# Kernel tuning notes

Hardware: AMD Instinct MI355X
Metric: run time of the kernel (lower is better)

Reference implementation:

```python
import jax, jax.numpy as jnp
import numpy as np
import math

B, C, N = 8, 512, 2048

def setup_inputs() -> dict:
    key = jax.random.key(0)
    ks = jax.random.split(key, 7)
    s = 0.02
    return {
        "x": jax.random.normal(ks[0], (B, C, N), dtype=jnp.float32),
        "Wq": jax.random.normal(ks[1], (C // 2, C), dtype=jnp.float32) * s,
        "bq": jax.random.normal(ks[2], (C // 2,), dtype=jnp.float32) * s,
        "Wk": jax.random.normal(ks[3], (C // 2, C), dtype=jnp.float32) * s,
        "bk": jax.random.normal(ks[4], (C // 2,), dtype=jnp.float32) * s,
        "Wv": jax.random.normal(ks[5], (C, C), dtype=jnp.float32) * s,
        "bv": jax.random.normal(ks[6], (C,), dtype=jnp.float32) * s,
    }

def reference(x, Wq, bq, Wk, bk, Wv, bv):
    # pointwise conv1d == channel matmul: (O,C) x (B,C,N) -> (B,O,N)
    Q = jnp.einsum('oc,bcn->bon', Wq, x) + bq[None, :, None]  # (B, C/2, N)
    K = jnp.einsum('oc,bcn->bon', Wk, x) + bk[None, :, None]  # (B, C/2, N)
    V = jnp.einsum('oc,bcn->bon', Wv, x) + bv[None, :, None]  # (B, C, N)
    scale = 1.0 / math.sqrt(K.shape[1])
    A = jnp.einsum('bcn,bcm->bnm', Q, K) * scale              # (B, N, N)
    A = jax.nn.softmax(A, axis=-1)
    out = jnp.einsum('bcm,bnm->bcn', V, A)                    # V @ A^T
    return x + out
```

## Files before the change

### kernel.cpp

```cpp
#include <hip/hip_runtime.h>

#define B_ 8
#define C_ 512
#define N_ 2048
#define O_ 256

typedef unsigned short u16;
typedef unsigned char u8;
typedef unsigned int uint;
typedef float f32x4 __attribute__((ext_vector_type(4)));
typedef int i32x8 __attribute__((ext_vector_type(8)));

#define AS1 __attribute__((address_space(1)))
#define AS3 __attribute__((address_space(3)))

__device__ __forceinline__ u16 f2bf(float f) {
  union { float f; unsigned u; } v; v.f = f;
  return (u16)((v.u + 0x7fffu + ((v.u >> 16) & 1u)) >> 16);
}
__device__ __forceinline__ float bf2f(u16 h) {
  union { uint u; float f; } v; v.u = ((uint)h) << 16; return v.f;
}
__device__ __forceinline__ uint pk4_e4m3(float a, float b, float c, float d) {
  int r = __builtin_amdgcn_cvt_pk_fp8_f32(a, b, 0, false);
  r = __builtin_amdgcn_cvt_pk_fp8_f32(c, d, r, true);
  return (uint)r;
}

union MxFrag { i32x8 v; uint4 q[2]; };

__device__ __forceinline__ void mx_mainloop(
    const u8* __restrict__ Ag, int lda,
    const u8* __restrict__ Bg, int ldb, int K,
    u8 (&As)[128][128], u8 (&Bs)[128][128], f32x4 (&acc)[4][4])
{
  const int t = threadIdx.x;
  const int lane = t & 63;
  const int w = t >> 6;
  const int wm = (w >> 1) * 64, wn = (w & 1) * 64;
  const int lrow = lane & 15, quad = lane >> 4;
  const int swz = lrow & 7;
  const int r8 = lane >> 3;
  const int gsrc = (lane & 7) ^ r8;

  for (int k0 = 0; k0 < K; k0 += 128) {
#pragma unroll
    for (int i = 0; i < 4; i++) {
      int row = i * 32 + w * 8;
      __builtin_amdgcn_global_load_lds(
          (const AS1 uint*)(Ag + (size_t)(row + r8) * lda + k0 + gsrc * 16),
          (AS3 uint*)(&As[row][0]), 16, 0, 0);
      __builtin_amdgcn_global_load_lds(
          (const AS1 uint*)(Bg + (size_t)(row + r8) * ldb + k0 + gsrc * 16),
          (AS3 uint*)(&Bs[row][0]), 16, 0, 0);
    }
    __syncthreads();
    const int g0 = (quad * 2) ^ swz, g1 = (quad * 2 + 1) ^ swz;
    MxFrag af[4], bfr[4];
#pragma unroll
    for (int i = 0; i < 4; i++) {
      const u8* rp = &As[wm + i * 16 + lrow][0];
      af[i].q[0] = *(const uint4*)(rp + g0 * 16);
      af[i].q[1] = *(const uint4*)(rp + g1 * 16);
    }
#pragma unroll
    for (int j = 0; j < 4; j++) {
      const u8* rp = &Bs[wn + j * 16 + lrow][0];
      bfr[j].q[0] = *(const uint4*)(rp + g0 * 16);
      bfr[j].q[1] = *(const uint4*)(rp + g1 * 16);
    }
#pragma unroll
    for (int i = 0; i < 4; i++)
#pragma unroll
      for (int j = 0; j < 4; j++)
        acc[i][j] = __builtin_amdgcn_mfma_scale_f32_16x16x128_f8f6f4(
            af[i].v, bfr[j].v, acc[i][j],
            0, 0,
            0, 0x7f7f7f7f,
            0, 0x7f7f7f7f);
    __syncthreads();
  }
}

__global__ __launch_bounds__(256) void prep_kernel(
    const float* __restrict__ x,
    const float* __restrict__ Wq, const float* __restrict__ Wk,
    const float* __restrict__ Wv,
    u8* __restrict__ xT8, u8* __restrict__ Wq8, u8* __restrict__ Wk8,
    u8* __restrict__ Wv8, float* __restrict__ rowsum)
{
  __shared__ u16 tile[64][72];
  const int bid = blockIdx.x;
  const int t = threadIdx.x;
  if (bid < 2048) {
    int b = bid >> 8;
    int n0 = (bid & 31) * 64;
    int c0 = ((bid >> 5) & 7) * 64;
    const float* src = x + (size_t)b * C_ * N_ + (size_t)c0 * N_ + n0;
    int r = t >> 4;
    int f4 = (t & 15) * 4;
#pragma unroll
    for (int i = 0; i < 4; i++) {
      int c = r + 16 * i;
      float4 v = *(const float4*)(src + (size_t)c * N_ + f4);
      tile[f4 + 0][c] = f2bf(v.x);
      tile[f4 + 1][c] = f2bf(v.y);
      tile[f4 + 2][c] = f2bf(v.z);
      tile[f4 + 3][c] = f2bf(v.w);
    }
    __syncthreads();
    u8* dst = xT8 + (size_t)b * N_ * C_ + (size_t)n0 * C_ + c0;
    int n = t >> 2;
    int cc = (t & 3) * 16;
    uint4 d;
    d.x = pk4_e4m3(bf2f(tile[n][cc + 0]), bf2f(tile[n][cc + 1]),
                   bf2f(tile[n][cc + 2]), bf2f(tile[n][cc + 3]));
    d.y = pk4_e4m3(bf2f(tile[n][cc + 4]), bf2f(tile[n][cc + 5]),
                   bf2f(tile[n][cc + 6]), bf2f(tile[n][cc + 7]));
    d.z = pk4_e4m3(bf2f(tile[n][cc + 8]), bf2f(tile[n][cc + 9]),
                   bf2f(tile[n][cc + 10]), bf2f(tile[n][cc + 11]));
    d.w = pk4_e4m3(bf2f(tile[n][cc + 12]), bf2f(tile[n][cc + 13]),
                   bf2f(tile[n][cc + 14]), bf2f(tile[n][cc + 15]));
    *(uint4*)(dst + (size_t)n * C_ + cc) = d;
  } else {
    int gid = (bid - 2048) * 256 + t;
    const float* src; u8* dst; int o;
    if (gid < 32768)      { src = Wq; dst = Wq8; o = gid; }
    else if (gid < 65536) { src = Wk; dst = Wk8; o = gid - 32768; }
    else                  { src = Wv; dst = Wv8; o = gid - 65536; }
    float4 v = *(const float4*)(src + (size_t)o * 4);
    *(uint*)(dst + (size_t)o * 4) = pk4_e4m3(v.x, v.y, v.z, v.w);
    if (gid < 4096) {
      float4 z = {0.f, 0.f, 0.f, 0.f};
      *(float4*)(rowsum + gid * 4) = z;
    }
  }
}

__global__ __launch_bounds__(256) void proj_all_kernel(
    const u8* __restrict__ xT8,
    const u8* __restrict__ Wq8, const float* __restrict__ bq,
    const u8* __restrict__ Wk8, const float* __restrict__ bk,
    const u8* __restrict__ Wv8, const float* __restrict__ bv,
    u8* __restrict__ Qt8, u8* __restrict__ Kt8, u8* __restrict__ V8)
{
  __shared__ __align__(16) u8 As[128][128], Bs[128][128];
  const int n0 = blockIdx.x * 128;
  const int b = blockIdx.y;
  const int sub = blockIdx.z;
  const u8* xTb = xT8 + (size_t)b * N_ * C_ + (size_t)n0 * C_;

  const f32x4 zero = {0.f, 0.f, 0.f, 0.f};
  f32x4 acc[4][4];
#pragma unroll
  for (int i = 0; i < 4; i++)
#pragma unroll
    for (int j = 0; j < 4; j++) acc[i][j] = zero;

  const int lane = threadIdx.x & 63;
  const int w = threadIdx.x >> 6;
  const int wm = (w >> 1) * 64, wn = (w & 1) * 64;
  const int quad = lane >> 4, lcol = lane & 15;

  if (sub < 4) {
    const int isK = sub >> 1;
    const int o0 = (sub & 1) * 128;
    const u8* Wg = (isK ? Wk8 : Wq8) + (size_t)o0 * C_;
    const float* bias = isK ? bk : bq;
    u8* outp = (isK ? Kt8 : Qt8) + (size_t)b * N_ * O_;

    mx_mainloop(Wg, C_, xTb, C_, C_, As, Bs, acc);

#pragma unroll
    for (int i = 0; i < 4; i++) {
      int obase = o0 + wm + i * 16 + quad * 4;
      float4 bb = *(const float4*)(bias + obase);
#pragma unroll
      for (int j = 0; j < 4; j++) {
        int n = n0 + wn + j * 16 + lcol;
        uint d = pk4_e4m3(acc[i][j][0] + bb.x, acc[i][j][1] + bb.y,
                          acc[i][j][2] + bb.z, acc[i][j][3] + bb.w);
        *(uint*)(outp + (size_t)n * O_ + obase) = d;
      }
    }
  } else {
    const int c0 = (sub - 4) * 128;
    const u8* Wg = Wv8 + (size_t)c0 * C_;
    u8* outp = V8 + (size_t)b * C_ * N_;

    mx_mainloop(xTb, C_, Wg, C_, C_, As, Bs, acc);

#pragma unroll
    for (int j = 0; j < 4; j++) {
      int c = c0 + wn + j * 16 + lcol;
      float bb = bv[c];
#pragma unroll
      for (int i = 0; i < 4; i++) {
        int nbase = n0 + wm + i * 16 + quad * 4;
        uint d = pk4_e4m3(acc[i][j][0] + bb, acc[i][j][1] + bb,
                          acc[i][j][2] + bb, acc[i][j][3] + bb);
        *(uint*)(outp + (size_t)c * N_ + nbase) = d;
      }
    }
  }
}

__global__ __launch_bounds__(256) void attn_s_kernel(
    const u8* __restrict__ Qt8, const u8* __restrict__ Kt8,
    u8* __restrict__ P, float* __restrict__ rowsum)
{
  __shared__ __align__(16) u8 As[128][128], Bs[128][128];
  int b = blockIdx.z;
  int m0 = blockIdx.x * 128, n0 = blockIdx.y * 128;
  const u8* Ag = Kt8 + (size_t)b * N_ * O_ + (size_t)m0 * O_;
  const u8* Bg = Qt8 + (size_t)b * N_ * O_ + (size_t)n0 * O_;

  const f32x4 zero = {0.f, 0.f, 0.f, 0.f};
  f32x4 acc[4][4];
#pragma unroll
  for (int i = 0; i < 4; i++)
#pragma unroll
    for (int j = 0; j < 4; j++) acc[i][j] = zero;

  mx_mainloop(Ag, O_, Bg, O_, O_, As, Bs, acc);

  u8* Pp = P + (size_t)b * N_ * N_;
  float* rs = rowsum + (size_t)b * N_;
  const int lane = threadIdx.x & 63;
  const int w = threadIdx.x >> 6;
  const int wm = (w >> 1) * 64, wn = (w & 1) * 64;
  const int quad = lane >> 4, lcol = lane & 15;

  float partial[4];
#pragma unroll
  for (int j = 0; j < 4; j++) partial[j] = 0.f;

#pragma unroll
  for (int j = 0; j < 4; j++) {
    int n = n0 + wn + j * 16 + lcol;
#pragma unroll
    for (int i = 0; i < 4; i++) {
      int mbase = m0 + wm + i * 16 + quad * 4;
      float p0 = __expf(acc[i][j][0] * 0.0625f);
      float p1 = __expf(acc[i][j][1] * 0.0625f);
      float p2 = __expf(acc[i][j][2] * 0.0625f);
      float p3 = __expf(acc[i][j][3] * 0.0625f);
      *(uint*)(Pp + (size_t)n * N_ + mbase) = pk4_e4m3(p0, p1, p2, p3);
      partial[j] += p0 + p1 + p2 + p3;
    }
  }
#pragma unroll
  for (int msk = 16; msk < 64; msk <<= 1)
#pragma unroll
    for (int j = 0; j < 4; j++)
      partial[j] += __shfl_xor(partial[j], msk);
  if (quad == 0) {
#pragma unroll
    for (int j = 0; j < 4; j++)
      atomicAdd(&rs[n0 + wn + j * 16 + lcol], partial[j]);
  }
}

__global__ __launch_bounds__(256) void attn_o_kernel(
    const u8* __restrict__ V, const u8* __restrict__ P,
    const float* __restrict__ rowsum, const float* __restrict__ x,
    float* __restrict__ out)
{
  __shared__ __align__(16) u8 As[64][128], Bs[128][128];
  const int b = blockIdx.z;
  const int c0 = blockIdx.y * 64, n0 = blockIdx.x * 128;
  const u8* Ag = V + (size_t)b * C_ * N_ + (size_t)c0 * N_;
  const u8* Bg = P + (size_t)b * N_ * N_ + (size_t)n0 * N_;

  const int t = threadIdx.x;
  const int lane = t & 63;
  const int w = t >> 6;
  const int wm = (w >> 1) * 32;
  const int wn = (w & 1) * 64;
  const int lrow = lane & 15, quad = lane >> 4;
  const int swz = lrow & 7;
  const int r8 = lane >> 3;
  const int gsrc = (lane & 7) ^ r8;

  const f32x4 zero = {0.f, 0.f, 0.f, 0.f};
  f32x4 acc[2][4];
#pragma unroll
  for (int i = 0; i < 2; i++)
#pragma unroll
    for (int j = 0; j < 4; j++) acc[i][j] = zero;

  for (int k0 = 0; k0 < N_; k0 += 128) {
#pragma unroll
    for (int s = 0; s < 2; s++) {
      int row = (w * 2 + s) * 8;
      __builtin_amdgcn_global_load_lds(
          (const AS1 uint*)(Ag + (size_t)(row + r8) * N_ + k0 + gsrc * 16),
          (AS3 uint*)(&As[row][0]), 16, 0, 0);
    }
#pragma unroll
    for (int s = 0; s < 4; s++) {
      int row = (w * 4 + s) * 8;
      __builtin_amdgcn_global_load_lds(
          (const AS1 uint*)(Bg + (size_t)(row + r8) * N_ + k0 + gsrc * 16),
          (AS3 uint*)(&Bs[row][0]), 16, 0, 0);
    }
    __syncthreads();
    const int g0 = (quad * 2) ^ swz, g1 = (quad * 2 + 1) ^ swz;
    MxFrag af[2], bfr[4];
#pragma unroll
    for (int i = 0; i < 2; i++) {
      const u8* rp = &As[wm + i * 16 + lrow][0];
      af[i].q[0] = *(const uint4*)(rp + g0 * 16);
      af[i].q[1] = *(const uint4*)(rp + g1 * 16);
    }
#pragma unroll
    for (int j = 0; j < 4; j++) {
      const u8* rp = &Bs[wn + j * 16 + lrow][0];
      bfr[j].q[0] = *(const uint4*)(rp + g0 * 16);
      bfr[j].q[1] = *(const uint4*)(rp + g1 * 16);
    }
#pragma unroll
    for (int i = 0; i < 2; i++)
#pragma unroll
      for (int j = 0; j < 4; j++)
        acc[i][j] = __builtin_amdgcn_mfma_scale_f32_16x16x128_f8f6f4(
            af[i].v, bfr[j].v, acc[i][j],
            0, 0, 0, 0x7f7f7f7f, 0, 0x7f7f7f7f);
    __syncthreads();
  }

  const float* xb = x + (size_t)b * C_ * N_;
  float* ob = out + (size_t)b * C_ * N_;
  float invl[4];
#pragma unroll
  for (int j = 0; j < 4; j++)
    invl[j] = 1.f / rowsum[b * N_ + n0 + wn + j * 16 + lrow];

#pragma unroll
  for (int i = 0; i < 2; i++)
#pragma unroll
    for (int rr = 0; rr < 4; rr++) {
      int c = c0 + wm + i * 16 + quad * 4 + rr;
#pragma unroll
      for (int j = 0; j < 4; j++) {
        int n = n0 + wn + j * 16 + lrow;
        size_t idx = (size_t)c * N_ + n;
        ob[idx] = xb[idx] + acc[i][j][rr] * invl[j];
      }
    }
}

extern "C" void kernel_launch(void* const* d_in, const int* in_sizes, int n_in,
                              void* d_out, int out_size, void* d_ws, size_t ws_size,
                              hipStream_t stream)
{
  (void)in_sizes; (void)n_in; (void)out_size; (void)ws_size;
  const float* x  = (const float*)d_in[0];
  const float* Wq = (const float*)d_in[1];
  const float* bq = (const float*)d_in[2];
  const float* Wk = (const float*)d_in[3];
  const float* bk = (const float*)d_in[4];
  const float* Wv = (const float*)d_in[5];
  const float* bv = (const float*)d_in[6];
  float* out = (float*)d_out;

  char* ws = (char*)d_ws;
  size_t off = 0;
  auto carve = [&](size_t bytes) -> char* {
    char* p = ws + off;
    off += (bytes + 255) & ~(size_t)255;
    return p;
  };
  u8*  xT8  = (u8*) carve((size_t)B_ * N_ * C_);
  u8*  Wq8  = (u8*) carve((size_t)O_ * C_);
  u8*  Wk8  = (u8*) carve((size_t)O_ * C_);
  u8*  Wv8  = (u8*) carve((size_t)C_ * C_);
  u8*  Qt8  = (u8*) carve((size_t)B_ * N_ * O_);
  u8*  Kt8  = (u8*) carve((size_t)B_ * N_ * O_);
  u8*  Vb   = (u8*) carve((size_t)B_ * C_ * N_);
  u8*  P    = (u8*) carve((size_t)B_ * N_ * N_);
  float* rowsum = (float*)carve((size_t)B_ * N_ * 4);

  prep_kernel<<<dim3(2560), 256, 0, stream>>>(
      x, Wq, Wk, Wv, xT8, Wq8, Wk8, Wv8, rowsum);
  proj_all_kernel<<<dim3(N_ / 128, B_, 8), 256, 0, stream>>>(
      xT8, Wq8, bq, Wk8, bk, Wv8, bv, Qt8, Kt8, Vb);
  attn_s_kernel<<<dim3(N_ / 128, N_ / 128, B_), 256, 0, stream>>>(Qt8, Kt8, P, rowsum);
  attn_o_kernel<<<dim3(N_ / 128, C_ / 64, B_), 256, 0, stream>>>(Vb, P, rowsum, x, out);
}
```

Measured before the change: 169.1 us.

## Double-buffer LDS tiles with async global-to-LDS prefetch in all GEMM kernels

Replaces the single-buffered load/sync/compute loops with a shared double-buffered mainloop. The next K tile is prefetched into LDS with global_load_lds while the current one is computed, using explicit vmcnt waits and raw barriers. This is meant to hide global memory latency behind MFMA work in the projection, score and output kernels. In exchange, LDS use per block doubles, which may lower occupancy, and correctness now depends on hand-placed waitcnt counts.

After: 177.5 us. 4.9% more time.

```diff
diff --git a/kernel.cpp b/kernel.cpp
--- a/kernel.cpp
+++ b/kernel.cpp
@@ -29,56 +29,91 @@
 
 union MxFrag { i32x8 v; uint4 q[2]; };
 
-__device__ __forceinline__ void mx_mainloop(
+template<int AR>
+__device__ __forceinline__ void mx_stage_tile(
     const u8* __restrict__ Ag, int lda,
-    const u8* __restrict__ Bg, int ldb, int K,
-    u8 (&As)[128][128], u8 (&Bs)[128][128], f32x4 (&acc)[4][4])
+    const u8* __restrict__ Bg, int ldb, int k0,
+    u8 (&As)[AR][128], u8 (&Bs)[128][128], int w, int r8, int gsrc)
+{
+#pragma unroll
+  for (int s = 0; s < AR / 32; s++) {
+    int row = (w * (AR / 32) + s) * 8;
+    __builtin_amdgcn_global_load_lds(
+        (const AS1 uint*)(Ag + (size_t)(row + r8) * lda + k0 + gsrc * 16),
+        (AS3 uint*)(&As[row][0]), 16, 0, 0);
+  }
+#pragma unroll
+  for (int s = 0; s < 4; s++) {
+    int row = (w * 4 + s) * 8;
+    __builtin_amdgcn_global_load_lds(
+        (const AS1 uint*)(Bg + (size_t)(row + r8) * ldb + k0 + gsrc * 16),
+        (AS3 uint*)(&Bs[row][0]), 16, 0, 0);
+  }
+}
+
+template<int MI, int AR>
+__device__ __forceinline__ void mx_compute_tile(
+    const u8 (&As)[AR][128], const u8 (&Bs)[128][128],
+    f32x4 (&acc)[MI][4], int wm, int wn, int lrow, int quad)
+{
+  const int swz = lrow & 7;
+  const int g0 = (quad * 2) ^ swz, g1 = (quad * 2 + 1) ^ swz;
+  MxFrag af[MI], bfr[4];
+#pragma unroll
+  for (int i = 0; i < MI; i++) {
+    const u8* rp = &As[wm + i * 16 + lrow][0];
+    af[i].q[0] = *(const uint4*)(rp + g0 * 16);
+    af[i].q[1] = *(const uint4*)(rp + g1 * 16);
+  }
+#pragma unroll
+  for (int j = 0; j < 4; j++) {
+    const u8* rp = &Bs[wn + j * 16 + lrow][0];
+    bfr[j].q[0] = *(const uint4*)(rp + g0 * 16);
+    bfr[j].q[1] = *(const uint4*)(rp + g1 * 16);
+  }
+  asm volatile("s_waitcnt lgkmcnt(0)" ::: "memory");
+#pragma unroll
+  for (int i = 0; i < MI; i++)
+#pragma unroll
+    for (int j = 0; j < 4; j++)
+      acc[i][j] = __builtin_amdgcn_mfma_scale_f32_16x16x128_f8f6f4(
+          af[i].v, bfr[j].v, acc[i][j],
+          0, 0,
+          0, 0x7f7f7f7f,
+          0, 0x7f7f7f7f);
+}
+
+template<int NT, int AR, int MI>
+__device__ __forceinline__ void mx_mainloop_db(
+    const u8* __restrict__ Ag, int lda,
+    const u8* __restrict__ Bg, int ldb,
+    u8 (&As)[2][AR][128], u8 (&Bs)[2][128][128],
+    f32x4 (&acc)[MI][4], int wm, int wn)
 {
   const int t = threadIdx.x;
   const int lane = t & 63;
   const int w = t >> 6;
-  const int wm = (w >> 1) * 64, wn = (w & 1) * 64;
   const int lrow = lane & 15, quad = lane >> 4;
-  const int swz = lrow & 7;
   const int r8 = lane >> 3;
   const int gsrc = (lane & 7) ^ r8;
-
-  for (int k0 = 0; k0 < K; k0 += 128) {
-#pragma unroll
-    for (int i = 0; i < 4; i++) {
-      int row = i * 32 + w * 8;
-      __builtin_amdgcn_global_load_lds(
-          (const AS1 uint*)(Ag + (size_t)(row + r8) * lda + k0 + gsrc * 16),
-          (AS3 uint*)(&As[row][0]), 16, 0, 0);
-      __builtin_amdgcn_global_load_lds(
-          (const AS1 uint*)(Bg + (size_t)(row + r8) * ldb + k0 + gsrc * 16),
-          (AS3 uint*)(&Bs[row][0]), 16, 0, 0);
-    }
-    __syncthreads();
-    const int g0 = (quad * 2) ^ swz, g1 = (quad * 2 + 1) ^ swz;
-    MxFrag af[4], bfr[4];
-#pragma unroll
-    for (int i = 0; i < 4; i++) {
-      const u8* rp = &As[wm + i * 16 + lrow][0];
-      af[i].q[0] = *(const uint4*)(rp + g0 * 16);
-      af[i].q[1] = *(const uint4*)(rp + g1 * 16);
-    }
-#pragma unroll
-    for (int j = 0; j < 4; j++) {
-      const u8* rp = &Bs[wn + j * 16 + lrow][0];
-      bfr[j].q[0] = *(const uint4*)(rp + g0 * 16);
-      bfr[j].q[1] = *(const uint4*)(rp + g1 * 16);
-    }
-#pragma unroll
-    for (int i = 0; i < 4; i++)
-#pragma unroll
-      for (int j = 0; j < 4; j++)
-        acc[i][j] = __builtin_amdgcn_mfma_scale_f32_16x16x128_f8f6f4(
-            af[i].v, bfr[j].v, acc[i][j],
-            0, 0,
-            0, 0x7f7f7f7f,
-            0, 0x7f7f7f7f);
-    __syncthreads();
+  constexpr int LPT = AR / 32 + 4;
+
+  mx_stage_tile<AR>(Ag, lda, Bg, ldb, 0, As[0], Bs[0], w, r8, gsrc);
+  if (NT > 1)
+    mx_stage_tile<AR>(Ag, lda, Bg, ldb, 128, As[1], Bs[1], w, r8, gsrc);
+
+#pragma unroll
+  for (int tt = 0; tt < NT; ++tt) {
+    if (tt + 1 < NT)
+      asm volatile("s_waitcnt vmcnt(%0)" :: "n"(LPT) : "memory");
+    else
+      asm volatile("s_waitcnt vmcnt(0)" ::: "memory");
+    __builtin_amdgcn_s_barrier();
+    mx_compute_tile<MI, AR>(As[tt & 1], Bs[tt & 1], acc, wm, wn, lrow, quad);
+    __builtin_amdgcn_s_barrier();
+    if (tt + 2 < NT)
+      mx_stage_tile<AR>(Ag, lda, Bg, ldb, (tt + 2) * 128,
+                        As[tt & 1], Bs[tt & 1], w, r8, gsrc);
   }
 }
 
@@ -144,7 +179,7 @@
     const u8* __restrict__ Wv8, const float* __restrict__ bv,
     u8* __restrict__ Qt8, u8* __restrict__ Kt8, u8* __restrict__ V8)
 {
-  __shared__ __align__(16) u8 As[128][128], Bs[128][128];
+  __shared__ __align__(16) u8 As[2][128][128], Bs[2][128][128];
   const int n0 = blockIdx.x * 128;
   const int b = blockIdx.y;
   const int sub = blockIdx.z;
@@ -169,7 +204,7 @@
     const float* bias = isK ? bk : bq;
     u8* outp = (isK ? Kt8 : Qt8) + (size_t)b * N_ * O_;
 
-    mx_mainloop(Wg, C_, xTb, C_, C_, As, Bs, acc);
+    mx_mainloop_db<4, 128, 4>(Wg, C_, xTb, C_, As, Bs, acc, wm, wn);
 
 #pragma unroll
     for (int i = 0; i < 4; i++) {
@@ -188,7 +223,7 @@
     const u8* Wg = Wv8 + (size_t)c0 * C_;
     u8* outp = V8 + (size_t)b * C_ * N_;
 
-    mx_mainloop(xTb, C_, Wg, C_, C_, As, Bs, acc);
+    mx_mainloop_db<4, 128, 4>(xTb, C_, Wg, C_, As, Bs, acc, wm, wn);
 
 #pragma unroll
     for (int j = 0; j < 4; j++) {
@@ -209,7 +244,7 @@
     const u8* __restrict__ Qt8, const u8* __restrict__ Kt8,
     u8* __restrict__ P, float* __restrict__ rowsum)
 {
-  __shared__ __align__(16) u8 As[128][128], Bs[128][128];
+  __shared__ __align__(16) u8 As[2][128][128], Bs[2][128][128];
   int b = blockIdx.z;
   int m0 = blockIdx.x * 128, n0 = blockIdx.y * 128;
   const u8* Ag = Kt8 + (size_t)b * N_ * O_ + (size_t)m0 * O_;
@@ -222,14 +257,15 @@
 #pragma unroll
     for (int j = 0; j < 4; j++) acc[i][j] = zero;
 
-  mx_mainloop(Ag, O_, Bg, O_, O_, As, Bs, acc);
-
-  u8* Pp = P + (size_t)b * N_ * N_;
-  float* rs = rowsum + (size_t)b * N_;
   const int lane = threadIdx.x & 63;
   const int w = threadIdx.x >> 6;
   const int wm = (w >> 1) * 64, wn = (w & 1) * 64;
   const int quad = lane >> 4, lcol = lane & 15;
+
+  mx_mainloop_db<2, 128, 4>(Ag, O_, Bg, O_, As, Bs, acc, wm, wn);
+
+  u8* Pp = P + (size_t)b * N_ * N_;
+  float* rs = rowsum + (size_t)b * N_;
 
   float partial[4];
 #pragma unroll
@@ -266,7 +302,7 @@
     const float* __restrict__ rowsum, const float* __restrict__ x,
     float* __restrict__ out)
 {
-  __shared__ __align__(16) u8 As[64][128], Bs[128][128];
+  __shared__ __align__(16) u8 As[2][64][128], Bs[2][128][128];
   const int b = blockIdx.z;
   const int c0 = blockIdx.y * 64, n0 = blockIdx.x * 128;
   const u8* Ag = V + (size_t)b * C_ * N_ + (size_t)c0 * N_;
@@ -278,9 +314,6 @@
   const int wm = (w >> 1) * 32;
   const int wn = (w & 1) * 64;
   const int lrow = lane & 15, quad = lane >> 4;
-  const int swz = lrow & 7;
-  const int r8 = lane >> 3;
-  const int gsrc = (lane & 7) ^ r8;
 
   const f32x4 zero = {0.f, 0.f, 0.f, 0.f};
   f32x4 acc[2][4];
@@ -289,45 +322,7 @@
 #pragma unroll
     for (int j = 0; j < 4; j++) acc[i][j] = zero;
 
-  for (int k0 = 0; k0 < N_; k0 += 128) {
-#pragma unroll
-    for (int s = 0; s < 2; s++) {
-      int row = (w * 2 + s) * 8;
-      __builtin_amdgcn_global_load_lds(
-          (const AS1 uint*)(Ag + (size_t)(row + r8) * N_ + k0 + gsrc * 16),
-          (AS3 uint*)(&As[row][0]), 16, 0, 0);
-    }
-#pragma unroll
-    for (int s = 0; s < 4; s++) {
-      int row = (w * 4 + s) * 8;
-      __builtin_amdgcn_global_load_lds(
-          (const AS1 uint*)(Bg + (size_t)(row + r8) * N_ + k0 + gsrc * 16),
-          (AS3 uint*)(&Bs[row][0]), 16, 0, 0);
-    }
-    __syncthreads();
-    const int g0 = (quad * 2) ^ swz, g1 = (quad * 2 + 1) ^ swz;
-    MxFrag af[2], bfr[4];
-#pragma unroll
-    for (int i = 0; i < 2; i++) {
-      const u8* rp = &As[wm + i * 16 + lrow][0];
-      af[i].q[0] = *(const uint4*)(rp + g0 * 16);
-      af[i].q[1] = *(const uint4*)(rp + g1 * 16);
-    }
-#pragma unroll
-    for (int j = 0; j < 4; j++) {
-      const u8* rp = &Bs[wn + j * 16 + lrow][0];
-      bfr[j].q[0] = *(const uint4*)(rp + g0 * 16);
-      bfr[j].q[1] = *(const uint4*)(rp + g1 * 16);
-    }
-#pragma unroll
-    for (int i = 0; i < 2; i++)
-#pragma unroll
-      for (int j = 0; j < 4; j++)
-        acc[i][j] = __builtin_amdgcn_mfma_scale_f32_16x16x128_f8f6f4(
-            af[i].v, bfr[j].v, acc[i][j],
-            0, 0, 0, 0x7f7f7f7f, 0, 0x7f7f7f7f);
-    __syncthreads();
-  }
+  mx_mainloop_db<16, 64, 2>(Ag, N_, Bg, N_, As, Bs, acc, wm, wn);
 
   const float* xb = x + (size_t)b * C_ * N_;
   float* ob = out + (size_t)b * C_ * N_;
```
